# Performance work log

Measured on AMD Instinct MI355X. Metric: run time of the kernel, lower is better.

## Reference

```python
import jax, jax.numpy as jnp
import numpy as np

N_NODES = 50000
N_EDGES = 1_600_000
N_REL = 8
D_IN = 128
D_OUT = 128


def _unique_edges(rng, n_nodes, n_rel, n_edges):
    # Torch module clamps the dense adjacency to 0/1, so duplicate
    # (rel, src, dst) triples collapse; generate unique edges so the
    # edge-list formulation matches exactly.
    m = 2 * n_edges
    src = rng.integers(0, n_nodes, m)
    dst = rng.integers(0, n_nodes, m)
    et = rng.integers(0, n_rel, m)
    key = (et.astype(np.int64) * n_nodes + src) * n_nodes + dst
    _, idx = np.unique(key, return_index=True)
    idx = np.sort(idx)[:n_edges]
    return src[idx], dst[idx], et[idx]


def setup_inputs() -> dict:
    key = jax.random.key(0)
    kx, kw, kr, kb = jax.random.split(key, 4)
    rng = np.random.default_rng(0)
    src, dst, et = _unique_edges(rng, N_NODES, N_REL, N_EDGES)
    bound = 1.0 / np.sqrt(D_OUT)
    return {
        "x": jax.random.normal(kx, (N_NODES, D_IN), dtype=jnp.float32),
        "edge_index": jnp.asarray(np.stack([src, dst]), dtype=jnp.int64),
        "edge_type": jnp.asarray(et, dtype=jnp.int64),
        "weight": jax.random.uniform(kw, (N_REL, D_OUT, D_IN), minval=-bound, maxval=bound, dtype=jnp.float32),
        "root": jax.random.uniform(kr, (D_OUT, D_IN), minval=-bound, maxval=bound, dtype=jnp.float32),
        "bias": jax.random.uniform(kb, (D_OUT,), minval=-bound, maxval=bound, dtype=jnp.float32),
    }


def reference(x, edge_index, edge_type, weight, root, bias):
    # Math identical to: adj[l, src, dst] = 1; adj row-normalized (mean);
    # out = sum_r norm_adj_r @ x @ W_r^T + x @ root^T + bias.
    n_rel, d_out, d_in = weight.shape
    n_nodes = x.shape[0]
    src = edge_index[0]
    dst = edge_index[1]
    seg = (edge_type * n_nodes + src).astype(jnp.int32)  # segment per (rel, node)
    num_seg = n_rel * n_nodes
    # sum of neighbor features per (relation, node): [R*N, d_in]
    agg = jax.ops.segment_sum(x[dst], seg, num_segments=num_seg)
    deg = jax.ops.segment_sum(jnp.ones((src.shape[0],), dtype=x.dtype), seg, num_segments=num_seg)
    norm = jnp.where(deg > 0, 1.0 / deg, 0.0)[:, None]  # mean aggr, nan_to_num(0)
    agg = (agg * norm).reshape(n_rel, n_nodes, d_in)
    out = jnp.einsum('rnd,rod->no', agg, weight)
    out = out + x @ root.T + bias[None]
    return out
```

## Files before the change

### kernel.cpp

```cpp
#include <hip/hip_runtime.h>


#define D 128
#define SCAN_CHUNK 2048
#define SEG_BITS 9
#define SEGS_PER_BUCKET 512
#define NBLK 128

typedef __attribute__((ext_vector_type(8))) short short8;
typedef __attribute__((ext_vector_type(4))) float v4f;

__device__ __forceinline__ unsigned short f2b(float f) {
    union { float f; unsigned u; } v; v.f = f;
    unsigned r = v.u + 0x7fffu + ((v.u >> 16) & 1u);
    return (unsigned short)(r >> 16);
}
__device__ __forceinline__ float blo(unsigned u) {
    union { unsigned u; float f; } v; v.u = u << 16; return v.f;
}
__device__ __forceinline__ float bhi(unsigned u) {
    union { unsigned u; float f; } v; v.u = u & 0xffff0000u; return v.f;
}

__global__ void cvt_bf16_all(const float* __restrict__ x, long long nx,
                             const float* __restrict__ w, long long nw,
                             const float* __restrict__ root, long long nr,
                             unsigned short* __restrict__ xB,
                             unsigned short* __restrict__ wB) {
    long long i = ((long long)blockIdx.x * blockDim.x + threadIdx.x) * 4;
    const float* src;
    unsigned short* dst;
    long long j;
    if (i < nx) { src = x; dst = xB; j = i; }
    else if (i < nx + nw) { src = w; dst = wB; j = i - nx; }
    else if (i < nx + nw + nr) { src = root; dst = wB + nw; j = i - nx - nw; }
    else return;
    float4 v = *(const float4*)(src + j);
    uint2 p;
    p.x = (unsigned)f2b(v.x) | ((unsigned)f2b(v.y) << 16);
    p.y = (unsigned)f2b(v.z) | ((unsigned)f2b(v.w) << 16);
    *(uint2*)(dst + j) = p;
}

__global__ __launch_bounds__(256)
void histA(const int* __restrict__ ei, const int* __restrict__ et,
           int* __restrict__ blockHist, int nE, int nN, int B, int epb) {
    __shared__ int lh[1024];
    const int tid = threadIdx.x;
    for (int b = tid; b < B; b += 256) lh[b] = 0;
    __syncthreads();
    const int base = blockIdx.x * epb;
    const int lim = min(base + epb, nE);
    for (int e = base + tid; e < lim; e += 256) {
        int seg = et[e] * nN + ei[e];
        atomicAdd(&lh[seg >> SEG_BITS], 1);
    }
    __syncthreads();
    for (int b = tid; b < B; b += 256)
        blockHist[b * NBLK + blockIdx.x] = lh[b];
}

__global__ __launch_bounds__(256)
void scan1(const int* __restrict__ in, int* __restrict__ excl,
           int* __restrict__ blockSums, int n) {
    __shared__ int t[256];
    const int tid = threadIdx.x;
    const int base = blockIdx.x * SCAN_CHUNK + tid * 8;
    int v[8];
    int tot = 0;
#pragma unroll
    for (int i = 0; i < 8; i++) {
        v[i] = (base + i < n) ? in[base + i] : 0;
        tot += v[i];
    }
    t[tid] = tot;
    __syncthreads();
    for (int off = 1; off < 256; off <<= 1) {
        int add = (tid >= off) ? t[tid - off] : 0;
        __syncthreads();
        t[tid] += add;
        __syncthreads();
    }
    int run = t[tid] - tot;
#pragma unroll
    for (int i = 0; i < 8; i++) {
        if (base + i < n) excl[base + i] = run;
        run += v[i];
    }
    if (tid == 255) blockSums[blockIdx.x] = t[255];
}

__global__ __launch_bounds__(256)
void scan2(int* __restrict__ blockSums, int nb) {
    __shared__ int t[256];
    const int tid = threadIdx.x;
    int v = (tid < nb) ? blockSums[tid] : 0;
    t[tid] = v;
    __syncthreads();
    for (int off = 1; off < 256; off <<= 1) {
        int add = (tid >= off) ? t[tid - off] : 0;
        __syncthreads();
        t[tid] += add;
        __syncthreads();
    }
    if (tid < nb) blockSums[tid] = t[tid] - v;
}

__global__ __launch_bounds__(256)
void scan3s(int* __restrict__ excl, const int* __restrict__ blockSums, int n) {
    const int base = blockIdx.x * SCAN_CHUNK + threadIdx.x * 8;
    const int bs = blockSums[blockIdx.x];
#pragma unroll
    for (int i = 0; i < 8; i++)
        if (base + i < n) excl[base + i] += bs;
}

__global__ __launch_bounds__(256)
void scatterA(const int* __restrict__ ei, const int* __restrict__ et,
              const int* __restrict__ scanned, unsigned* __restrict__ bucketEdges,
              int nE, int nN, int B, int epb) {
    __shared__ int cur[1024];
    const int tid = threadIdx.x;
    for (int b = tid; b < B; b += 256) cur[b] = scanned[b * NBLK + blockIdx.x];
    __syncthreads();
    const int base = blockIdx.x * epb;
    const int lim = min(base + epb, nE);
    for (int e = base + tid; e < lim; e += 256) {
        int seg = et[e] * nN + ei[e];
        int bkt = seg >> SEG_BITS;
        unsigned pk = ((unsigned)(seg & (SEGS_PER_BUCKET - 1)) << 16) | (unsigned)ei[nE + e];
        int pos = atomicAdd(&cur[bkt], 1);
        bucketEdges[pos] = pk;
    }
}

__global__ __launch_bounds__(256)
void segOff(const unsigned* __restrict__ bucketEdges, const int* __restrict__ scanned,
            int* __restrict__ off, unsigned short* __restrict__ sortedDst,
            int nE, int numSeg, int B) {
    __shared__ int lh[SEGS_PER_BUCKET];
    __shared__ int sc[256];
    __shared__ int lcur[SEGS_PER_BUCKET];
    const int tid = threadIdx.x;
    const int b = blockIdx.x;
    const int eBase = scanned[b * NBLK];
    const int eEnd = (b + 1 < B) ? scanned[(b + 1) * NBLK] : nE;
    const int segBase = b * SEGS_PER_BUCKET;
    const int segLim = min(SEGS_PER_BUCKET, numSeg - segBase);

    lh[2 * tid] = 0; lh[2 * tid + 1] = 0;
    __syncthreads();
    for (int i = eBase + tid; i < eEnd; i += 256)
        atomicAdd(&lh[bucketEdges[i] >> 16], 1);
    __syncthreads();
    int a0 = lh[2 * tid], a1 = lh[2 * tid + 1];
    sc[tid] = a0 + a1;
    __syncthreads();
    for (int o = 1; o < 256; o <<= 1) {
        int add = (tid >= o) ? sc[tid - o] : 0;
        __syncthreads();
        sc[tid] += add;
        __syncthreads();
    }
    int pairBase = sc[tid] - (a0 + a1);
    int g0 = eBase + pairBase;
    int g1 = g0 + a0;
    lcur[2 * tid] = g0;
    lcur[2 * tid + 1] = g1;
    if (2 * tid < segLim)     off[segBase + 2 * tid] = g0;
    if (2 * tid + 1 < segLim) off[segBase + 2 * tid + 1] = g1;
    if (b == B - 1 && tid == 0) off[numSeg] = nE;
    __syncthreads();
    for (int i = eBase + tid; i < eEnd; i += 256) {
        unsigned u = bucketEdges[i];
        int pos = atomicAdd(&lcur[u >> 16], 1);
        sortedDst[pos] = (unsigned short)(u & 0xFFFFu);
    }
}

__global__ __launch_bounds__(256)
void rgcn_gather(const unsigned short* __restrict__ xB,
                 const unsigned short* __restrict__ sortedDst,
                 const int* __restrict__ off,
                 unsigned short* __restrict__ aggB, int nN) {
    const int tid = threadIdx.x;
    const int lane = tid & 63;
    const int idx16 = lane & 15;
    const int grp = lane >> 4;
    const int wv = tid >> 6;
    const int n = blockIdx.x * 16 + wv * 4 + grp;
    const int r = blockIdx.y;
    const bool valid = (n < nN);
    const int seg = valid ? (r * nN + n) : 0;

    const int start = off[seg];
    int cnt = valid ? (off[seg + 1] - start) : 0;

    int mx = cnt;
    mx = max(mx, __shfl_xor(mx, 16));
    mx = max(mx, __shfl_xor(mx, 32));

    float2 acc2[4];
#pragma unroll
    for (int i = 0; i < 4; i++) acc2[i] = make_float2(0.f, 0.f);

    const unsigned short* xChunk = xB + idx16 * 8;

    for (int b = 0; b < mx; b += 16) {
        int myDst = (b + idx16 < cnt) ? (int)sortedDst[start + b + idx16] : 0;
        int kcap = min(16, mx - b);
        for (int k = 0; k < kcap; k++) {
            int dst = __shfl(myDst, grp * 16 + k);
            if (b + k < cnt) {
                uint4 v = *(const uint4*)(xChunk + ((size_t)dst << 7));
                acc2[0].x += blo(v.x); acc2[0].y += bhi(v.x);
                acc2[1].x += blo(v.y); acc2[1].y += bhi(v.y);
                acc2[2].x += blo(v.z); acc2[2].y += bhi(v.z);
                acc2[3].x += blo(v.w); acc2[3].y += bhi(v.w);
            }
        }
    }

    if (valid) {
        float s = cnt > 0 ? 1.0f / (float)cnt : 0.f;
        uint4 pkt;
        pkt.x = (unsigned)f2b(acc2[0].x * s) | ((unsigned)f2b(acc2[0].y * s) << 16);
        pkt.y = (unsigned)f2b(acc2[1].x * s) | ((unsigned)f2b(acc2[1].y * s) << 16);
        pkt.z = (unsigned)f2b(acc2[2].x * s) | ((unsigned)f2b(acc2[2].y * s) << 16);
        pkt.w = (unsigned)f2b(acc2[3].x * s) | ((unsigned)f2b(acc2[3].y * s) << 16);
        *(uint4*)(aggB + ((size_t)seg) * D + idx16 * 8) = pkt;
    }
}

#define APITCH 72
__global__ __launch_bounds__(256)
void rgcn_gemm_mfma(const unsigned short* __restrict__ aggB,
                    const unsigned short* __restrict__ xB,
                    const unsigned short* __restrict__ wB,
                    const float* __restrict__ bias,
                    float* __restrict__ out, int nN, int nRel) {
    __shared__ __align__(16) unsigned short As[64 * APITCH];
    __shared__ __align__(16) unsigned short Bs[128 * APITCH];
    const int tid = threadIdx.x;
    const int wave = tid >> 6;
    const int lane = tid & 63;
    const int wm = wave & 1;
    const int wn = wave >> 1;
    const int m16 = lane & 15;
    const int q = lane >> 4;
    const int row0 = blockIdx.x * 64;

    v4f acc[2][4];
#pragma unroll
    for (int i = 0; i < 2; i++)
#pragma unroll
        for (int j = 0; j < 4; j++) acc[i][j] = (v4f){0.f, 0.f, 0.f, 0.f};

    const int nSlabs = nRel + 1;
    for (int s = 0; s < nSlabs; s++) {
        const unsigned short* aSrc = (s < nRel) ? (aggB + (size_t)s * nN * D) : xB;
        const unsigned short* bSrc = wB + (size_t)s * D * D;
        for (int h = 0; h < 2; h++) {
            const int dbase = h * 64;
#pragma unroll
            for (int p = 0; p < 2; p++) {
                int idx = tid + p * 256;
                int arow = idx >> 3;
                int ch = idx & 7;
                int n = row0 + arow;
                uint4 v = make_uint4(0u, 0u, 0u, 0u);
                if (n < nN)
                    v = *(const uint4*)(aSrc + (size_t)n * D + dbase + ch * 8);
                *(uint4*)&As[arow * APITCH + ch * 8] = v;
            }
#pragma unroll
            for (int p = 0; p < 4; p++) {
                int idx = tid + p * 256;
                int o = idx >> 3;
                int ch = idx & 7;
                uint4 v = *(const uint4*)(bSrc + (size_t)o * D + dbase + ch * 8);
                *(uint4*)&Bs[o * APITCH + ch * 8] = v;
            }
            __syncthreads();

#pragma unroll
            for (int kb = 0; kb < 64; kb += 32) {
                short8 a[2], b[4];
#pragma unroll
                for (int mt = 0; mt < 2; mt++)
                    a[mt] = *(const short8*)&As[(wm * 32 + mt * 16 + m16) * APITCH + kb + q * 8];
#pragma unroll
                for (int nt = 0; nt < 4; nt++)
                    b[nt] = *(const short8*)&Bs[(wn * 64 + nt * 16 + m16) * APITCH + kb + q * 8];
#pragma unroll
                for (int mt = 0; mt < 2; mt++)
#pragma unroll
                    for (int nt = 0; nt < 4; nt++)
                        acc[mt][nt] = __builtin_amdgcn_mfma_f32_16x16x32_bf16(
                            a[mt], b[nt], acc[mt][nt], 0, 0, 0);
            }
            __syncthreads();
        }
    }

#pragma unroll
    for (int mt = 0; mt < 2; mt++) {
#pragma unroll
        for (int nt = 0; nt < 4; nt++) {
            int col = wn * 64 + nt * 16 + m16;
            float bi = bias[col];
#pragma unroll
            for (int reg = 0; reg < 4; reg++) {
                int rrow = row0 + wm * 32 + mt * 16 + q * 4 + reg;
                if (rrow < nN)
                    out[(size_t)rrow * D + col] = acc[mt][nt][reg] + bi;
            }
        }
    }
}

extern "C" void kernel_launch(void* const* d_in, const int* in_sizes, int n_in,
                              void* d_out, int out_size, void* d_ws, size_t ws_size,
                              hipStream_t stream) {
    const float* x    = (const float*)d_in[0];
    const int*   ei   = (const int*)d_in[1];
    const int*   et   = (const int*)d_in[2];
    const float* w    = (const float*)d_in[3];
    const float* root = (const float*)d_in[4];
    const float* bias = (const float*)d_in[5];
    float* out = (float*)d_out;

    const int nN   = in_sizes[0] / D;
    const int nE   = in_sizes[2];
    const int nRel = in_sizes[3] / (D * D);
    const int numSeg = nRel * nN;
    const int B = (numSeg + SEGS_PER_BUCKET - 1) >> SEG_BITS;
    const int nBH = B * NBLK;
    const int epb = (nE + NBLK - 1) / NBLK;

    char* p = (char*)d_ws;
    unsigned* bucketEdges   = (unsigned*)p;        p += (size_t)nE * sizeof(unsigned);
    unsigned short* sortedDst = (unsigned short*)p; p += (size_t)nE * sizeof(unsigned short);
    p = (char*)(((uintptr_t)p + 255) & ~(uintptr_t)255);
    int* off       = (int*)p;  p += (size_t)(numSeg + 1) * sizeof(int);
    int* blockHist = (int*)p;  p += (size_t)nBH * sizeof(int);
    int* scanned   = (int*)p;  p += (size_t)nBH * sizeof(int);
    int* blockSums = (int*)p;  p += 256 * sizeof(int);
    p = (char*)(((uintptr_t)p + 255) & ~(uintptr_t)255);
    unsigned short* xB   = (unsigned short*)p;  p += (size_t)nN * D * sizeof(unsigned short);
    unsigned short* wB   = (unsigned short*)p;  p += (size_t)(nRel + 1) * D * D * sizeof(unsigned short);
    p = (char*)(((uintptr_t)p + 255) & ~(uintptr_t)255);
    unsigned short* aggB = (unsigned short*)p;

    const int nScanBlocks = (nBH + SCAN_CHUNK - 1) / SCAN_CHUNK;

    histA<<<NBLK, 256, 0, stream>>>(ei, et, blockHist, nE, nN, B, epb);
    scan1<<<nScanBlocks, 256, 0, stream>>>(blockHist, scanned, blockSums, nBH);
    scan2<<<1, 256, 0, stream>>>(blockSums, nScanBlocks);
    scan3s<<<nScanBlocks, 256, 0, stream>>>(scanned, blockSums, nBH);
    scatterA<<<NBLK, 256, 0, stream>>>(ei, et, scanned, bucketEdges, nE, nN, B, epb);
    segOff<<<B, 256, 0, stream>>>(bucketEdges, scanned, off, sortedDst, nE, numSeg, B);

    long long nx = (long long)nN * D;
    long long nw = (long long)nRel * D * D;
    long long nr = (long long)D * D;
    long long ncvt = (nx + nw + nr) / 4;
    cvt_bf16_all<<<(int)((ncvt + 255) / 256), 256, 0, stream>>>(x, nx, w, nw, root, nr, xB, wB);

    dim3 gg((nN + 15) / 16, nRel);
    rgcn_gather<<<gg, 256, 0, stream>>>(xB, sortedDst, off, aggB, nN);

    rgcn_gemm_mfma<<<(nN + 63) / 64, 256, 0, stream>>>(aggB, xB, wB, bias, out, nN, nRel);
}
```

Before: 275.6 us.

## Fuse neighbor gather into MFMA GEMM, aggregating directly into shared memory

Merges the separate gather and GEMM kernels: each 64-row block now computes the per-relation mean aggregation straight into an LDS A-tile (full 128-wide pitch), then runs the MFMA against that relation's weights. This removes the round trip of the aggregated bf16 tensor (R*N*128) through global memory and one kernel launch. In exchange the grid shrinks to about 782 blocks with gather and MFMA phases serialized inside each block, so latency hiding for the irregular gathers depends on occupancy (launch bounds 256,4) and load imbalance across rows.

After: 297.3 us. 7.9% more time.

```diff
diff --git a/kernel.cpp b/kernel.cpp
--- a/kernel.cpp
+++ b/kernel.cpp
@@ -6,6 +6,8 @@
 #define SEG_BITS 9
 #define SEGS_PER_BUCKET 512
 #define NBLK 128
+#define AP 136
+#define BP 72
 
 typedef __attribute__((ext_vector_type(8))) short short8;
 typedef __attribute__((ext_vector_type(4))) float v4f;
@@ -178,74 +180,22 @@
     }
 }
 
-__global__ __launch_bounds__(256)
-void rgcn_gather(const unsigned short* __restrict__ xB,
-                 const unsigned short* __restrict__ sortedDst,
-                 const int* __restrict__ off,
-                 unsigned short* __restrict__ aggB, int nN) {
-    const int tid = threadIdx.x;
+__global__ __launch_bounds__(256, 4)
+void rgcn_fused_mfma(const unsigned short* __restrict__ xB,
+                     const unsigned short* __restrict__ sortedDst,
+                     const int* __restrict__ off,
+                     const unsigned short* __restrict__ wB,
+                     const float* __restrict__ bias,
+                     float* __restrict__ out, int nN, int nRel) {
+    __shared__ __align__(16) unsigned short As[64 * AP];
+    __shared__ __align__(16) unsigned short Bs[128 * BP];
+    const int tid = threadIdx.x;
+    const int wv = tid >> 6;
     const int lane = tid & 63;
     const int idx16 = lane & 15;
     const int grp = lane >> 4;
-    const int wv = tid >> 6;
-    const int n = blockIdx.x * 16 + wv * 4 + grp;
-    const int r = blockIdx.y;
-    const bool valid = (n < nN);
-    const int seg = valid ? (r * nN + n) : 0;
-
-    const int start = off[seg];
-    int cnt = valid ? (off[seg + 1] - start) : 0;
-
-    int mx = cnt;
-    mx = max(mx, __shfl_xor(mx, 16));
-    mx = max(mx, __shfl_xor(mx, 32));
-
-    float2 acc2[4];
-#pragma unroll
-    for (int i = 0; i < 4; i++) acc2[i] = make_float2(0.f, 0.f);
-
-    const unsigned short* xChunk = xB + idx16 * 8;
-
-    for (int b = 0; b < mx; b += 16) {
-        int myDst = (b + idx16 < cnt) ? (int)sortedDst[start + b + idx16] : 0;
-        int kcap = min(16, mx - b);
-        for (int k = 0; k < kcap; k++) {
-            int dst = __shfl(myDst, grp * 16 + k);
-            if (b + k < cnt) {
-                uint4 v = *(const uint4*)(xChunk + ((size_t)dst << 7));
-                acc2[0].x += blo(v.x); acc2[0].y += bhi(v.x);
-                acc2[1].x += blo(v.y); acc2[1].y += bhi(v.y);
-                acc2[2].x += blo(v.z); acc2[2].y += bhi(v.z);
-                acc2[3].x += blo(v.w); acc2[3].y += bhi(v.w);
-            }
-        }
-    }
-
-    if (valid) {
-        float s = cnt > 0 ? 1.0f / (float)cnt : 0.f;
-        uint4 pkt;
-        pkt.x = (unsigned)f2b(acc2[0].x * s) | ((unsigned)f2b(acc2[0].y * s) << 16);
-        pkt.y = (unsigned)f2b(acc2[1].x * s) | ((unsigned)f2b(acc2[1].y * s) << 16);
-        pkt.z = (unsigned)f2b(acc2[2].x * s) | ((unsigned)f2b(acc2[2].y * s) << 16);
-        pkt.w = (unsigned)f2b(acc2[3].x * s) | ((unsigned)f2b(acc2[3].y * s) << 16);
-        *(uint4*)(aggB + ((size_t)seg) * D + idx16 * 8) = pkt;
-    }
-}
-
-#define APITCH 72
-__global__ __launch_bounds__(256)
-void rgcn_gemm_mfma(const unsigned short* __restrict__ aggB,
-                    const unsigned short* __restrict__ xB,
-                    const unsigned short* __restrict__ wB,
-                    const float* __restrict__ bias,
-                    float* __restrict__ out, int nN, int nRel) {
-    __shared__ __align__(16) unsigned short As[64 * APITCH];
-    __shared__ __align__(16) unsigned short Bs[128 * APITCH];
-    const int tid = threadIdx.x;
-    const int wave = tid >> 6;
-    const int lane = tid & 63;
-    const int wm = wave & 1;
-    const int wn = wave >> 1;
+    const int wm = wv & 1;
+    const int wn = wv >> 1;
     const int m16 = lane & 15;
     const int q = lane >> 4;
     const int row0 = blockIdx.x * 64;
@@ -256,30 +206,72 @@
 #pragma unroll
         for (int j = 0; j < 4; j++) acc[i][j] = (v4f){0.f, 0.f, 0.f, 0.f};
 
-    const int nSlabs = nRel + 1;
-    for (int s = 0; s < nSlabs; s++) {
-        const unsigned short* aSrc = (s < nRel) ? (aggB + (size_t)s * nN * D) : xB;
+    const unsigned short* xChunk = xB + idx16 * 8;
+
+    for (int s = 0; s <= nRel; s++) {
+        __syncthreads();
+        if (s < nRel) {
+#pragma unroll 1
+            for (int it = 0; it < 4; it++) {
+                const int arow = wv * 16 + it * 4 + grp;
+                const int n = row0 + arow;
+                const bool valid = (n < nN);
+                const int seg = valid ? (s * nN + n) : 0;
+                const int start = off[seg];
+                int cnt = valid ? (off[seg + 1] - start) : 0;
+                int mx = cnt;
+                mx = max(mx, __shfl_xor(mx, 16));
+                mx = max(mx, __shfl_xor(mx, 32));
+                float2 acc2[4];
+#pragma unroll
+                for (int i = 0; i < 4; i++) acc2[i] = make_float2(0.f, 0.f);
+                for (int b = 0; b < mx; b += 16) {
+                    int myDst = (b + idx16 < cnt) ? (int)sortedDst[start + b + idx16] : 0;
+                    int kcap = min(16, mx - b);
+                    for (int k = 0; k < kcap; k++) {
+                        int dst = __shfl(myDst, grp * 16 + k);
+                        if (b + k < cnt) {
+                            uint4 v = *(const uint4*)(xChunk + ((size_t)dst << 7));
+                            acc2[0].x += blo(v.x); acc2[0].y += bhi(v.x);
+                            acc2[1].x += blo(v.y); acc2[1].y += bhi(v.y);
+                            acc2[2].x += blo(v.z); acc2[2].y += bhi(v.z);
+                            acc2[3].x += blo(v.w); acc2[3].y += bhi(v.w);
+                        }
+                    }
+                }
+                float sc = cnt > 0 ? 1.0f / (float)cnt : 0.f;
+                uint4 pkt;
+                pkt.x = (unsigned)f2b(acc2[0].x * sc) | ((unsigned)f2b(acc2[0].y * sc) << 16);
+                pkt.y = (unsigned)f2b(acc2[1].x * sc) | ((unsigned)f2b(acc2[1].y * sc) << 16);
+                pkt.z = (unsigned)f2b(acc2[2].x * sc) | ((unsigned)f2b(acc2[2].y * sc) << 16);
+                pkt.w = (unsigned)f2b(acc2[3].x * sc) | ((unsigned)f2b(acc2[3].y * sc) << 16);
+                *(uint4*)&As[arow * AP + idx16 * 8] = pkt;
+            }
+        } else {
+#pragma unroll
+            for (int p2 = 0; p2 < 4; p2++) {
+                int idx = tid + p2 * 256;
+                int arow = idx >> 4;
+                int ch = idx & 15;
+                int n = row0 + arow;
+                uint4 v = make_uint4(0u, 0u, 0u, 0u);
+                if (n < nN)
+                    v = *(const uint4*)(xB + (size_t)n * D + ch * 8);
+                *(uint4*)&As[arow * AP + ch * 8] = v;
+            }
+        }
+
         const unsigned short* bSrc = wB + (size_t)s * D * D;
         for (int h = 0; h < 2; h++) {
             const int dbase = h * 64;
-#pragma unroll
-            for (int p = 0; p < 2; p++) {
-                int idx = tid + p * 256;
-                int arow = idx >> 3;
-                int ch = idx & 7;
-                int n = row0 + arow;
-                uint4 v = make_uint4(0u, 0u, 0u, 0u);
-                if (n < nN)
-                    v = *(const uint4*)(aSrc + (size_t)n * D + dbase + ch * 8);
-                *(uint4*)&As[arow * APITCH + ch * 8] = v;
-            }
-#pragma unroll
-            for (int p = 0; p < 4; p++) {
-                int idx = tid + p * 256;
+            __syncthreads();
+#pragma unroll
+            for (int p2 = 0; p2 < 4; p2++) {
+                int idx = tid + p2 * 256;
                 int o = idx >> 3;
                 int ch = idx & 7;
                 uint4 v = *(const uint4*)(bSrc + (size_t)o * D + dbase + ch * 8);
-                *(uint4*)&Bs[o * APITCH + ch * 8] = v;
+                *(uint4*)&Bs[o * BP + ch * 8] = v;
             }
             __syncthreads();
 
@@ -288,10 +280,10 @@
                 short8 a[2], b[4];
 #pragma unroll
                 for (int mt = 0; mt < 2; mt++)
-                    a[mt] = *(const short8*)&As[(wm * 32 + mt * 16 + m16) * APITCH + kb + q * 8];
+                    a[mt] = *(const short8*)&As[(wm * 32 + mt * 16 + m16) * AP + dbase + kb + q * 8];
 #pragma unroll
                 for (int nt = 0; nt < 4; nt++)
-                    b[nt] = *(const short8*)&Bs[(wn * 64 + nt * 16 + m16) * APITCH + kb + q * 8];
+                    b[nt] = *(const short8*)&Bs[(wn * 64 + nt * 16 + m16) * BP + kb + q * 8];
 #pragma unroll
                 for (int mt = 0; mt < 2; mt++)
 #pragma unroll
@@ -299,7 +291,6 @@
                         acc[mt][nt] = __builtin_amdgcn_mfma_f32_16x16x32_bf16(
                             a[mt], b[nt], acc[mt][nt], 0, 0, 0);
             }
-            __syncthreads();
         }
     }
 
@@ -349,8 +340,6 @@
     p = (char*)(((uintptr_t)p + 255) & ~(uintptr_t)255);
     unsigned short* xB   = (unsigned short*)p;  p += (size_t)nN * D * sizeof(unsigned short);
     unsigned short* wB   = (unsigned short*)p;  p += (size_t)(nRel + 1) * D * D * sizeof(unsigned short);
-    p = (char*)(((uintptr_t)p + 255) & ~(uintptr_t)255);
-    unsigned short* aggB = (unsigned short*)p;
 
     const int nScanBlocks = (nBH + SCAN_CHUNK - 1) / SCAN_CHUNK;
 
@@ -367,8 +356,6 @@
     long long ncvt = (nx + nw + nr) / 4;
     cvt_bf16_all<<<(int)((ncvt + 255) / 256), 256, 0, stream>>>(x, nx, w, nw, root, nr, xB, wB);
 
-    dim3 gg((nN + 15) / 16, nRel);
-    rgcn_gather<<<gg, 256, 0, stream>>>(xB, sortedDst, off, aggB, nN);
-
-    rgcn_gemm_mfma<<<(nN + 63) / 64, 256, 0, stream>>>(aggB, xB, wB, bias, out, nN, nRel);
-}
+    rgcn_fused_mfma<<<(nN + 63) / 64, 256, 0, stream>>>(xB, sortedDst, off, wB, bias,
+                                                        out, nN, nRel);
+}
```
